# Optimization experiments

Measured on AMD Instinct MI355X. Metric: run time of the kernel, lower is better.

The kernel has to match this reference:

```python
import jax, jax.numpy as jnp
import numpy as np

B, S, D, H, W1, G = 2, 4096, 768, 12, 256, 8  # W1 = one-sided window (attention_window // 2)
HD = D // H
NC = S // W1  # number of query chunks of size W1
NEG = -1e9


def setup_inputs():
    key = jax.random.key(0)
    ks = jax.random.split(key, 9)
    def w(k):
        return jax.random.normal(k, (D, D), jnp.float32) * 0.02
    zb = jnp.zeros((D,), jnp.float32)
    # mask: >0 global, 0 local, <0 masked. First G tokens are global.
    mask = jnp.zeros((B, 1, 1, S), jnp.int32).at[:, :, :, :G].set(1)
    return {
        "hidden_states": jax.random.normal(ks[0], (B, S, D), jnp.float32),
        "attention_mask": mask,
        "Wq": w(ks[1]), "bq": zb,
        "Wk": w(ks[2]), "bk": zb,
        "Wv": w(ks[3]), "bv": zb,
        "Wqg": w(ks[4]), "bqg": zb,
        "Wkg": w(ks[5]), "bkg": zb,
        "Wvg": w(ks[6]), "bvg": zb,
        "Wo": w(ks[7]), "bo": zb,
        "n_global": G,
    }


def reference(hidden_states, attention_mask, Wq, bq, Wk, bk, Wv, bv,
              Wqg, bqg, Wkg, bkg, Wvg, bvg, Wo, bo, n_global):
    g = n_global
    mask = attention_mask.reshape(B, S)
    key_neg = mask < 0  # masked-out positions
    scale = 1.0 / np.sqrt(HD)

    def heads(x):  # [B,S,D] -> [B,H,S,HD]
        return x.reshape(B, S, H, HD).transpose(0, 2, 1, 3)

    q = heads(hidden_states @ Wq + bq) * scale
    k = heads(hidden_states @ Wk + bk)
    v = heads(hidden_states @ Wv + bv)

    # ---- sliding-window (banded) scores via 3-chunk gather ----
    idx = jnp.arange(NC)[:, None] * W1 + jnp.arange(3 * W1)[None, :]  # [NC,3W] into padded seq
    k_ch = jnp.pad(k, ((0, 0), (0, 0), (W1, W1), (0, 0)))[:, :, idx]  # [B,H,NC,3W,HD]
    q_ch = q.reshape(B, H, NC, W1, HD)
    band = jnp.einsum('bhcqd,bhckd->bhcqk', q_ch, k_ch)  # [B,H,NC,W,3W]

    qi = jnp.arange(W1)
    kj = jnp.arange(3 * W1)
    band_ok = jnp.abs(kj[None, :] - W1 - qi[:, None]) <= W1        # [W,3W] |j-i|<=w
    j_abs = idx - W1                                               # absolute key index
    in_range = (j_abs >= 0) & (j_abs < S)                          # [NC,3W]
    neg_ch = jnp.pad(key_neg, ((0, 0), (W1, W1)))[:, idx]          # [B,NC,3W]
    valid = (band_ok[None, None, None]
             & in_range[None, None, :, None, :]
             & (~neg_ch)[:, None, :, None, :])                     # [B,1,NC,W,3W]
    band = jnp.where(valid, band, NEG)

    # ---- scores of every query against the global keys (regular k proj) ----
    glob = jnp.einsum('bhsd,bhgd->bhsg', q, k[:, :, :g])           # [B,H,S,G]
    glob = jnp.where(key_neg[:, None, None, :g], NEG, glob)

    scores = jnp.concatenate([glob.reshape(B, H, NC, W1, g), band], axis=-1)
    probs = jax.nn.softmax(scores, axis=-1)
    probs = jnp.where(key_neg.reshape(B, 1, NC, W1, 1), 0.0, probs)  # zero masked query rows

    v_ch = jnp.pad(v, ((0, 0), (0, 0), (W1, W1), (0, 0)))[:, :, idx]
    out = jnp.einsum('bhcqk,bhckd->bhcqd', probs[..., g:], v_ch)
    out = out + jnp.einsum('bhcqg,bhgd->bhcqd', probs[..., :g], v[:, :, :g])
    out = out.reshape(B, H, S, HD)

    # ---- global tokens: full attention with dedicated global projections ----
    qg = heads(hidden_states @ Wqg + bqg)[:, :, :g] * scale        # [B,H,G,HD]
    kg = heads(hidden_states @ Wkg + bkg)
    vg = heads(hidden_states @ Wvg + bvg)
    gs = jnp.einsum('bhgd,bhsd->bhgs', qg, kg)                     # [B,H,G,S]
    gs = jnp.where(key_neg[:, None, None, :], NEG, gs)
    gp = jax.nn.softmax(gs, axis=-1)
    og = jnp.einsum('bhgs,bhsd->bhgd', gp, vg)
    out = out.at[:, :, :g].set(og)

    merged = out.transpose(0, 2, 1, 3).reshape(B, S, D)
    return merged @ Wo + bo  # outer output projection
```

## Files before the change

kernel.cpp:

```cpp
#include <hip/hip_runtime.h>

#define BB 2
#define SS 4096
#define DD 768
#define HH 12
#define HDD 64
#define W1C 256
#define NCC 16
#define GG 8

typedef unsigned short u16;
typedef __attribute__((ext_vector_type(4))) unsigned short u16x4;
typedef __attribute__((ext_vector_type(8))) unsigned short u16x8;
typedef __attribute__((ext_vector_type(8))) short s16x8;
typedef __attribute__((ext_vector_type(4))) float f32x4;

__device__ __forceinline__ float b2f(u16 u) {
  union { unsigned int i; float f; } v;
  v.i = ((unsigned int)u) << 16;
  return v.f;
}
__device__ __forceinline__ u16 f2b(float f) {
  union { float f; unsigned int i; } v;
  v.f = f;
  unsigned int r = v.i + 0x7FFFu + ((v.i >> 16) & 1u);
  return (u16)(r >> 16);
}
__device__ __forceinline__ float fexp2(float x) {
#if __has_builtin(__builtin_amdgcn_exp2f)
  return __builtin_amdgcn_exp2f(x);
#else
  return exp2f(x);
#endif
}
__device__ __forceinline__ unsigned pk_bf16(float lo, float hi) {
  unsigned r;
  asm("v_cvt_pk_bf16_f32 %0, %1, %2" : "=v"(r) : "v"(lo), "v"(hi));
  return r;
}
__device__ __forceinline__ void load_lds16(const void* g, void* l) {
  __builtin_amdgcn_global_load_lds(
      (const __attribute__((address_space(1))) unsigned int*)g,
      (__attribute__((address_space(3))) unsigned int*)l, 16, 0, 0);
}

#define QSCALE 0.18033688011112042f

__global__ __launch_bounds__(256) void cvt_f32_bf16(
    const float* __restrict__ in, u16* __restrict__ out, int n8) {
  int i = blockIdx.x * 256 + threadIdx.x;
  if (i >= n8) return;
  const float4* p = (const float4*)(in + (size_t)i * 8);
  float4 a = p[0], b = p[1];
  u16x8 o;
  o[0] = f2b(a.x); o[1] = f2b(a.y); o[2] = f2b(a.z); o[3] = f2b(a.w);
  o[4] = f2b(b.x); o[5] = f2b(b.y); o[6] = f2b(b.z); o[7] = f2b(b.w);
  *(u16x8*)(out + (size_t)i * 8) = o;
}

struct WtArgs { const float* W[6]; };

__global__ __launch_bounds__(256) void transpose_wt(WtArgs wa,
                                                    u16* __restrict__ WT) {
  __shared__ float T[64][65];
  const int mat = blockIdx.z;
  const int k0 = blockIdx.y * 64;
  const int n0 = blockIdx.x * 64;
  const float* __restrict__ W = wa.W[mat];
  const int t = threadIdx.x;
#pragma unroll
  for (int i = 0; i < 4; i++) {
    int idx4 = t + i * 256;
    int r = idx4 >> 4, c4 = idx4 & 15;
    float4 v = *(const float4*)(W + (size_t)(k0 + r) * 768 + n0 + c4 * 4);
    T[r][c4 * 4 + 0] = v.x; T[r][c4 * 4 + 1] = v.y;
    T[r][c4 * 4 + 2] = v.z; T[r][c4 * 4 + 3] = v.w;
  }
  __syncthreads();
#pragma unroll
  for (int i = 0; i < 2; i++) {
    int ci = t + i * 256;
    int nl = ci >> 3, k8 = ci & 7;
    u16x8 o;
#pragma unroll
    for (int jj = 0; jj < 8; jj++) o[jj] = f2b(T[k8 * 8 + jj][nl]);
    *(u16x8*)(WT + ((size_t)mat * 768 + n0 + nl) * 768 + k0 + k8 * 8) = o;
  }
}

struct BiasArgs { const float* bias[5]; };

template <int MODE>
__global__ __launch_bounds__(256) void gemm_bf16(
    const u16* __restrict__ A, const u16* __restrict__ WT, BiasArgs ba,
    u16* __restrict__ outb, float* __restrict__ outf) {
  __shared__ __align__(16) u16 As[128 * 64];
  __shared__ __align__(16) u16 Bs[128 * 64];
  const int tid = threadIdx.x;
  const int w = tid >> 6, l = tid & 63;
  const int lq = l & 15, g = l >> 4;

  const int NB = (MODE == 0) ? 30 : 6;
  const int nwg = NB * 64;
  const int cpx = nwg >> 3;
  const int id = (int)blockIdx.x;
  const int swz = (id & 7) * cpx + (id >> 3);
  const int bn = swz % NB, bm = swz / NB;

  const int m0 = bm * 128;
  const int wsel = (MODE == 0) ? (bn / 6) : 0;
  const int n0 = (MODE == 0) ? ((bn % 6) * 128) : (bn * 128);
  const int nw0 = bn * 128;
  const float* __restrict__ bias = ba.bias[wsel];
  const int wm = w >> 1, wn = w & 1;

  f32x4 acc[4][4];
#pragma unroll
  for (int i = 0; i < 4; i++)
#pragma unroll
    for (int j = 0; j < 4; j++) acc[i][j] = (f32x4){0.f, 0.f, 0.f, 0.f};

  for (int k0 = 0; k0 < 768; k0 += 64) {
    __syncthreads();
#pragma unroll
    for (int j = 0; j < 4; j++) {
      const int ci = (j * 4 + w) * 64 + l;
      const int row = ci >> 3, sl = ci & 7;
      const int src = sl ^ (row & 7);
      load_lds16(A + (size_t)(m0 + row) * 768 + k0 + src * 8,
                 (char*)As + (j * 4 + w) * 1024);
    }
#pragma unroll
    for (int j = 0; j < 4; j++) {
      const int ci = (j * 4 + w) * 64 + l;
      const int row = ci >> 3, sl = ci & 7;
      const int src = sl ^ (row & 7);
      load_lds16(WT + (size_t)(nw0 + row) * 768 + k0 + src * 8,
                 (char*)Bs + (j * 4 + w) * 1024);
    }
    asm volatile("s_waitcnt vmcnt(0)" ::: "memory");
    __syncthreads();
#pragma unroll
    for (int s = 0; s < 2; s++) {
      s16x8 af[4], bf[4];
#pragma unroll
      for (int mi = 0; mi < 4; mi++) {
        const int r = wm * 64 + mi * 16 + lq;
        af[mi] = *(const s16x8*)(As + r * 64 + (((s * 4 + g) ^ (r & 7)) * 8));
      }
#pragma unroll
      for (int nj = 0; nj < 4; nj++) {
        const int r = wn * 64 + nj * 16 + lq;
        bf[nj] = *(const s16x8*)(Bs + r * 64 + (((s * 4 + g) ^ (r & 7)) * 8));
      }
#pragma unroll
      for (int mi = 0; mi < 4; mi++)
#pragma unroll
        for (int nj = 0; nj < 4; nj++)
          acc[mi][nj] = __builtin_amdgcn_mfma_f32_16x16x32_bf16(
              af[mi], bf[nj], acc[mi][nj], 0, 0, 0);
    }
  }

  const int rbase = g * 4;
  const int cl = lq;
  if (MODE == 0) {
    const float scale = (wsel == 0) ? QSCALE : 1.0f;
    u16* outw = outb + (size_t)wsel * ((size_t)BB * HH * SS * HDD);
#pragma unroll
    for (int nj = 0; nj < 4; nj++) {
      const int c = n0 + wn * 64 + nj * 16 + cl;
      const float bv = bias[c];
      const int h = c >> 6, hd = c & 63;
#pragma unroll
      for (int mi = 0; mi < 4; mi++) {
#pragma unroll
        for (int r = 0; r < 4; r++) {
          const int m = m0 + wm * 64 + mi * 16 + rbase + r;
          const int b = m >> 12, s = m & 4095;
          outw[((size_t)(b * HH + h) * SS + s) * HDD + hd] =
              f2b((acc[mi][nj][r] + bv) * scale);
        }
      }
    }
  } else {
#pragma unroll
    for (int nj = 0; nj < 4; nj++) {
      const int c = n0 + wn * 64 + nj * 16 + cl;
      const float bv = bias[c];
#pragma unroll
      for (int mi = 0; mi < 4; mi++) {
#pragma unroll
        for (int r = 0; r < 4; r++) {
          const int m = m0 + wm * 64 + mi * 16 + rbase + r;
          outf[(size_t)m * 768 + c] = acc[mi][nj][r] + bv;
        }
      }
    }
  }
}

__global__ __launch_bounds__(256) void qg_proj(
    const float* __restrict__ hs, const float* __restrict__ Wqg,
    const float* __restrict__ bqg, u16* __restrict__ QG) {
  __shared__ float hsL[8][768];
  const int bh = blockIdx.x;
  const int b = bh / HH, h = bh % HH;
  const int t = threadIdx.x;
#pragma unroll
  for (int i = 0; i < 6; i++) {
    int idx = t + i * 256;
    int row = idx / 192, c4 = idx % 192;
    *(float4*)&hsL[row][c4 * 4] =
        *(const float4*)(hs + ((size_t)b * SS + row) * DD + c4 * 4);
  }
  __syncthreads();
#pragma unroll
  for (int rep = 0; rep < 2; rep++) {
    int qi = rep * 4 + (t >> 6);
    int d = t & 63, n = h * 64 + d;
    float acc = bqg[n];
    for (int k = 0; k < DD; k++)
      acc = fmaf(hsL[qi][k], Wqg[(size_t)k * DD + n], acc);
    QG[((size_t)bh * 16 + qi) * 64 + d] = f2b(acc * QSCALE);
  }
#pragma unroll
  for (int i = 0; i < 2; i++) {
    int idx = t + i * 256;
    int row = 8 + (idx >> 6), d = idx & 63;
    QG[((size_t)bh * 16 + row) * 64 + d] = 0;
  }
}

template <int GLOBAL>
__global__ __launch_bounds__(256) void attn_mfma(
    const u16* __restrict__ Q, const u16* __restrict__ K,
    const u16* __restrict__ V, const int* __restrict__ amask,
    u16* __restrict__ ATT, float* __restrict__ Pnum,
    float* __restrict__ Pden) {
  extern __shared__ __align__(16) char smem[];
  const int tid = threadIdx.x;
  const int w = tid >> 6, lane = tid & 63;
  const int lq = lane & 15, g = lane >> 4;
  const int h = blockIdx.y, b = blockIdx.z;
  const int bh = b * HH + h;
  const size_t bhs = (size_t)bh * SS;
  const int q0 = GLOBAL ? 0 : (int)blockIdx.x * 64;
  const int split = GLOBAL ? (int)blockIdx.x : 0;

  char* Kl;
  char* VT;
  if constexpr (GLOBAL) {
    Kl = smem + w * 16384;
    VT = Kl + 8192;
  } else {
    Kl = smem;
    VT = smem + 8192;
  }

  s16x8 qf[2];
  {
    const u16* qp = GLOBAL ? (Q + ((size_t)bh * 16 + lq) * 64)
                           : (Q + (bhs + q0 + w * 16 + lq) * 64);
    qf[0] = *(const s16x8*)(qp + g * 8);
    qf[1] = *(const s16x8*)(qp + 32 + g * 8);
  }

  f32x4 oacc[4];
#pragma unroll
  for (int i = 0; i < 4; i++) oacc[i] = (f32x4){0.f, 0.f, 0.f, 0.f};
  float denom = 0.f;

  const int NT = GLOBAL ? 2 : 10;
  for (int kt = 0; kt < NT; kt++) {
    int j0, klimit;
    bool bandfree;
    if constexpr (GLOBAL) {
      j0 = split * 512 + (w * 2 + kt) * 64;
      bandfree = true;
      klimit = 64;
    } else {
      if (kt < 9) { j0 = q0 - 256 + kt * 64; bandfree = false; klimit = 64; }
      else        { j0 = 0;                  bandfree = true;  klimit = 8; }
    }

    int jm = j0 + lane;
    int mv = ((unsigned)jm < (unsigned)SS) ? amask[b * SS + jm] : -1;
    bool okk = (mv >= 0) && (lane < klimit);
    unsigned long long vm = __ballot(okk);

    if constexpr (GLOBAL) {
      asm volatile("s_waitcnt lgkmcnt(0)" ::: "memory");
      const u16* Ks = K + bhs * 64 + (size_t)j0 * 64;
#pragma unroll
      for (int i = 0; i < 8; i++) {
        int ci = i * 64 + lane;
        int row = ci >> 3, cc = ci & 7, cs = cc ^ (row & 7);
        load_lds16(Ks + row * 64 + cs * 8, Kl + i * 1024);
      }
      const u16* Vs = V + bhs * 64 + (size_t)j0 * 64;
#pragma unroll
      for (int p = 0; p < 8; p++) {
        u16x8 vv = *(const u16x8*)(Vs + (size_t)lane * 64 + p * 8);
#pragma unroll
        for (int e = 0; e < 8; e++)
          *(u16*)(VT + (p * 8 + e) * 128 + ((lane * 2) ^ (e << 4))) = vv[e];
      }
      asm volatile("s_waitcnt vmcnt(0) lgkmcnt(0)" ::: "memory");
    } else {
      __syncthreads();
      if (j0 >= 0 && j0 + 64 <= SS) {
        const u16* Ks = K + bhs * 64 + (size_t)j0 * 64;
#pragma unroll
        for (int i = 0; i < 2; i++) {
          int ci = (i * 4 + w) * 64 + lane;
          int row = ci >> 3, cc = ci & 7, cs = cc ^ (row & 7);
          load_lds16(Ks + row * 64 + cs * 8, Kl + (i * 4 + w) * 1024);
        }
      } else {
#pragma unroll
        for (int i = 0; i < 2; i++) {
          int ci = (i * 4 + w) * 64 + lane;
          int row = ci >> 3, cc = ci & 7, cs = cc ^ (row & 7);
          int jj = j0 + row;
          u16x8 val;
#pragma unroll
          for (int e = 0; e < 8; e++) val[e] = 0;
          if ((unsigned)jj < (unsigned)SS)
            val = *(const u16x8*)(K + (bhs + jj) * 64 + cs * 8);
          *(u16x8*)(Kl + ci * 16) = val;
        }
      }
#pragma unroll
      for (int p = 0; p < 2; p++) {
        int d0 = p * 32 + w * 8;
        int jj = j0 + lane;
        u16x8 vv;
#pragma unroll
        for (int e = 0; e < 8; e++) vv[e] = 0;
        if ((unsigned)jj < (unsigned)SS)
          vv = *(const u16x8*)(V + (bhs + jj) * 64 + d0);
#pragma unroll
        for (int e = 0; e < 8; e++)
          *(u16*)(VT + (d0 + e) * 128 + ((lane * 2) ^ (e << 4))) = vv[e];
      }
      asm volatile("s_waitcnt vmcnt(0)" ::: "memory");
      __syncthreads();
    }

    f32x4 sc[4];
#pragma unroll
    for (int i = 0; i < 4; i++) sc[i] = (f32x4){0.f, 0.f, 0.f, 0.f};
#pragma unroll
    for (int s = 0; s < 2; s++) {
#pragma unroll
      for (int ks = 0; ks < 4; ks++) {
        s16x8 kf = *(const s16x8*)(Kl + (ks * 16 + lq) * 128 +
                                   (((s * 4 + g) ^ (lq & 7)) << 4));
        sc[ks] = __builtin_amdgcn_mfma_f32_16x16x32_bf16(kf, qf[s], sc[ks],
                                                          0, 0, 0);
      }
    }

    {
      const unsigned mlo = (unsigned)vm, mhi = (unsigned)(vm >> 32);
      const int q_abs = q0 + w * 16 + lq;
      bool allin = bandfree;
      if constexpr (!GLOBAL) {
        const int qw = q0 + w * 16;
        allin = bandfree || (j0 >= qw - 241 && j0 <= qw + 193);
      }
      const bool fast = (vm == ~0ull) && allin;
      const int ddq = j0 + g * 4 - q_abs;
      const int gsh = g * 4;
      if (fast) {
#pragma unroll
        for (int ks = 0; ks < 4; ks++)
#pragma unroll
          for (int r = 0; r < 4; r++) {
            float p = fexp2(sc[ks][r]);
            sc[ks][r] = p;
            denom += p;
          }
      } else {
#pragma unroll
        for (int ks = 0; ks < 4; ks++)
#pragma unroll
          for (int r = 0; r < 4; r++) {
            float e = fexp2(sc[ks][r]);
            unsigned bit =
                ((ks < 2 ? mlo : mhi) >> (gsh + ((ks & 1) * 16 + r))) & 1u;
            bool ok = bit && (allin ||
                              (unsigned)(ddq + ks * 16 + r + 256) <= 512u);
            float p = ok ? e : 0.f;
            sc[ks][r] = p;
            denom += p;
          }
      }
    }

#pragma unroll
    for (int s = 0; s < 2; s++) {
      const int srcA = lq + ((g & 1) << 5);
      const bool hiSel = g >= 2;
      float L[4], H[4];
#pragma unroll
      for (int r = 0; r < 4; r++) {
        float a0 = __shfl(sc[2 * s][r], srcA);
        float a1 = __shfl(sc[2 * s + 1][r], srcA);
        L[r] = hiSel ? a1 : a0;
        float b0 = __shfl(sc[2 * s][r], srcA + 16);
        float b1 = __shfl(sc[2 * s + 1][r], srcA + 16);
        H[r] = hiSel ? b1 : b0;
      }
      union { unsigned u[4]; s16x8 v; } pf;
      pf.u[0] = pk_bf16(L[0], L[1]);
      pf.u[1] = pk_bf16(L[2], L[3]);
      pf.u[2] = pk_bf16(H[0], H[1]);
      pf.u[3] = pk_bf16(H[2], H[3]);
#pragma unroll
      for (int dblk = 0; dblk < 4; dblk++) {
        s16x8 vf = *(const s16x8*)(VT + (dblk * 16 + lq) * 128 +
                                   (((s * 4 + g) ^ (lq & 7)) << 4));
        oacc[dblk] = __builtin_amdgcn_mfma_f32_16x16x32_bf16(vf, pf.v,
                                                              oacc[dblk],
                                                              0, 0, 0);
      }
    }
  }

  denom += __shfl_xor(denom, 16);
  denom += __shfl_xor(denom, 32);
  if constexpr (!GLOBAL) {
    const int q_abs = q0 + w * 16 + lq;
    const float rowscale = (amask[b * SS + q_abs] >= 0) ? (1.f / denom) : 0.f;
    u16* orow = ATT + ((size_t)b * SS + q_abs) * DD + h * 64;
#pragma unroll
    for (int dblk = 0; dblk < 4; dblk++) {
      u16x4 o;
#pragma unroll
      for (int r = 0; r < 4; r++) o[r] = f2b(oacc[dblk][r] * rowscale);
      *(u16x4*)(orow + dblk * 16 + g * 4) = o;
    }
  } else {
    const int pidx = split * 4 + w;
    float* np = Pnum + ((size_t)bh * 32 + pidx) * 1024;
#pragma unroll
    for (int dblk = 0; dblk < 4; dblk++)
#pragma unroll
      for (int r = 0; r < 4; r++)
        np[(dblk * 16 + g * 4 + r) * 16 + lq] = oacc[dblk][r];
    Pden[((size_t)bh * 32 + pidx) * 16 + lq] = denom;
  }
}

__global__ __launch_bounds__(512) void gmerge(const float* __restrict__ Pnum,
                                              const float* __restrict__ Pden,
                                              u16* __restrict__ ATT) {
  const int bh = blockIdx.x;
  const int b = bh / HH, h = bh % HH;
  const int t = threadIdx.x;
  const int q = t >> 6, d = t & 63;
  float num = 0.f, den = 0.f;
#pragma unroll 4
  for (int p = 0; p < 32; p++) {
    num += Pnum[((size_t)bh * 32 + p) * 1024 + d * 16 + q];
    den += Pden[((size_t)bh * 32 + p) * 16 + q];
  }
  ATT[((size_t)b * SS + q) * DD + h * 64 + d] = f2b(num / den);
}

extern "C" void kernel_launch(void* const* d_in, const int* in_sizes, int n_in,
                              void* d_out, int out_size, void* d_ws,
                              size_t ws_size, hipStream_t stream) {
  const float* hs = (const float*)d_in[0];
  const int* amask = (const int*)d_in[1];
  const float* Wq = (const float*)d_in[2];
  const float* bq = (const float*)d_in[3];
  const float* Wk = (const float*)d_in[4];
  const float* bk = (const float*)d_in[5];
  const float* Wv = (const float*)d_in[6];
  const float* bv = (const float*)d_in[7];
  const float* Wqg = (const float*)d_in[8];
  const float* bqg = (const float*)d_in[9];
  const float* Wkg = (const float*)d_in[10];
  const float* bkg = (const float*)d_in[11];
  const float* Wvg = (const float*)d_in[12];
  const float* bvg = (const float*)d_in[13];
  const float* Wo = (const float*)d_in[14];
  const float* bo = (const float*)d_in[15];
  float* out = (float*)d_out;

  char* ws = (char*)d_ws;
  const size_t QSZB = (size_t)BB * HH * SS * HDD * 2;
  u16* Qb = (u16*)(ws + 0);
  u16* Kb = (u16*)(ws + QSZB);
  u16* Vb = (u16*)(ws + 2 * QSZB);
  u16* KGb = (u16*)(ws + 3 * QSZB);
  u16* VGb = (u16*)(ws + 4 * QSZB);
  u16* Ab = (u16*)(ws + 5 * QSZB);
  u16* WTb = (u16*)(ws + 6 * QSZB);
  u16* ATTb = (u16*)(ws + 6 * QSZB + 7077888);
  u16* QGb = (u16*)(ws + 7 * QSZB + 7077888);
  float* Pnum = (float*)(ws + 7 * QSZB + 7077888 + 49152);
  float* Pden = (float*)(ws + 7 * QSZB + 7077888 + 49152 + 3145728);

  hipLaunchKernelGGL(cvt_f32_bf16, dim3(3072), dim3(256), 0, stream, hs, Ab,
                     (int)((size_t)BB * SS * DD / 8));

  WtArgs wa;
  wa.W[0] = Wq; wa.W[1] = Wk; wa.W[2] = Wv;
  wa.W[3] = Wkg; wa.W[4] = Wvg; wa.W[5] = Wo;
  hipLaunchKernelGGL(transpose_wt, dim3(12, 12, 6), dim3(256), 0, stream, wa,
                     WTb);

  BiasArgs b0;
  b0.bias[0] = bq; b0.bias[1] = bk; b0.bias[2] = bv;
  b0.bias[3] = bkg; b0.bias[4] = bvg;
  hipLaunchKernelGGL((gemm_bf16<0>), dim3(1920), dim3(256), 0, stream, Ab,
                     WTb, b0, Qb, (float*)nullptr);

  hipLaunchKernelGGL(qg_proj, dim3(24), dim3(256), 0, stream, hs, Wqg, bqg,
                     QGb);

  hipLaunchKernelGGL((attn_mfma<1>), dim3(8, HH, BB), dim3(256), 65536,
                     stream, QGb, KGb, VGb, amask, (u16*)nullptr, Pnum, Pden);

  hipLaunchKernelGGL((attn_mfma<0>), dim3(64, HH, BB), dim3(256), 16384,
                     stream, Qb, Kb, Vb, amask, ATTb, (float*)nullptr,
                     (float*)nullptr);

  hipLaunchKernelGGL(gmerge, dim3(24), dim3(512), 0, stream, Pnum, Pden, ATTb);

  BiasArgs b1;
  for (int i = 0; i < 5; i++) b1.bias[i] = bo;
  hipLaunchKernelGGL((gemm_bf16<1>), dim3(384), dim3(256), 0, stream, ATTb,
                     WTb + (size_t)5 * 768 * 768, b1, (u16*)nullptr, out);
}
```

Measured before the change: 208.9 us.

## Double-buffer bf16 GEMM with larger 256x256 tiles and 512-thread blocks

```diff
diff --git a/kernel.cpp b/kernel.cpp
--- a/kernel.cpp
+++ b/kernel.cpp
@@ -91,92 +91,149 @@
 struct BiasArgs { const float* bias[5]; };
 
 template <int MODE>
-__global__ __launch_bounds__(256) void gemm_bf16(
+__global__ __launch_bounds__(512, 1) void gemm_bf16(
     const u16* __restrict__ A, const u16* __restrict__ WT, BiasArgs ba,
     u16* __restrict__ outb, float* __restrict__ outf) {
-  __shared__ __align__(16) u16 As[128 * 64];
-  __shared__ __align__(16) u16 Bs[128 * 64];
+  constexpr int BM = (MODE == 0) ? 256 : 128;
+  constexpr int WM = BM / 2;
+  constexpr int MHAL = BM / 128;
+  constexpr int ATILE = BM * 64 * 2;
+  constexpr int BTILE = 256 * 64 * 2;
+  constexpr int BUFB = ATILE + BTILE;
+  constexpr int ACH = ATILE / 1024;
+  constexpr int ALD = ACH / 8;
+  constexpr int NTL = (MODE == 0) ? 15 : 3;
+  constexpr int NWG = (MODE == 0) ? 480 : 192;
+  constexpr int NT = 12;
+
+  extern __shared__ __align__(16) char smem[];
+
   const int tid = threadIdx.x;
   const int w = tid >> 6, l = tid & 63;
   const int lq = l & 15, g = l >> 4;
-
-  const int NB = (MODE == 0) ? 30 : 6;
-  const int nwg = NB * 64;
-  const int cpx = nwg >> 3;
+  const int wm = w >> 2, wn = w & 3;
+
+  const int cpx = NWG >> 3;
   const int id = (int)blockIdx.x;
   const int swz = (id & 7) * cpx + (id >> 3);
-  const int bn = swz % NB, bm = swz / NB;
-
-  const int m0 = bm * 128;
-  const int wsel = (MODE == 0) ? (bn / 6) : 0;
-  const int n0 = (MODE == 0) ? ((bn % 6) * 128) : (bn * 128);
-  const int nw0 = bn * 128;
+  const int bm = swz / NTL, bn = swz % NTL;
+  const int m0 = bm * BM;
+  const int nw0 = bn * 256;
+  const int wsel = (MODE == 0) ? (bn / 3) : 0;
+  const int nmat0 = (MODE == 0) ? ((bn % 3) * 256) : (bn * 256);
   const float* __restrict__ bias = ba.bias[wsel];
-  const int wm = w >> 1, wn = w & 1;
-
-  f32x4 acc[4][4];
-#pragma unroll
-  for (int i = 0; i < 4; i++)
+
+  f32x4 acc[MHAL * 4][4];
+#pragma unroll
+  for (int i = 0; i < MHAL * 4; i++)
 #pragma unroll
     for (int j = 0; j < 4; j++) acc[i][j] = (f32x4){0.f, 0.f, 0.f, 0.f};
 
-  for (int k0 = 0; k0 < 768; k0 += 64) {
-    __syncthreads();
+  auto stage = [&](int t) {
+    const int k0 = t * 64;
+    char* uA = smem + (t & 1) * BUFB;
+    char* uB = uA + ATILE;
+#pragma unroll
+    for (int j = 0; j < ALD; j++) {
+      const int ci = j * 8 + w;
+      const int p = ci * 64 + l;
+      const int row = p >> 3, sl = p & 7;
+      load_lds16(A + (size_t)(m0 + row) * 768 + k0 + ((sl ^ (row & 7)) * 8),
+                 uA + ci * 1024);
+    }
 #pragma unroll
     for (int j = 0; j < 4; j++) {
-      const int ci = (j * 4 + w) * 64 + l;
-      const int row = ci >> 3, sl = ci & 7;
-      const int src = sl ^ (row & 7);
-      load_lds16(A + (size_t)(m0 + row) * 768 + k0 + src * 8,
-                 (char*)As + (j * 4 + w) * 1024);
-    }
-#pragma unroll
-    for (int j = 0; j < 4; j++) {
-      const int ci = (j * 4 + w) * 64 + l;
-      const int row = ci >> 3, sl = ci & 7;
-      const int src = sl ^ (row & 7);
-      load_lds16(WT + (size_t)(nw0 + row) * 768 + k0 + src * 8,
-                 (char*)Bs + (j * 4 + w) * 1024);
-    }
-    asm volatile("s_waitcnt vmcnt(0)" ::: "memory");
-    __syncthreads();
-#pragma unroll
-    for (int s = 0; s < 2; s++) {
-      s16x8 af[4], bf[4];
-#pragma unroll
-      for (int mi = 0; mi < 4; mi++) {
-        const int r = wm * 64 + mi * 16 + lq;
-        af[mi] = *(const s16x8*)(As + r * 64 + (((s * 4 + g) ^ (r & 7)) * 8));
-      }
-#pragma unroll
-      for (int nj = 0; nj < 4; nj++) {
-        const int r = wn * 64 + nj * 16 + lq;
-        bf[nj] = *(const s16x8*)(Bs + r * 64 + (((s * 4 + g) ^ (r & 7)) * 8));
-      }
-#pragma unroll
-      for (int mi = 0; mi < 4; mi++)
-#pragma unroll
-        for (int nj = 0; nj < 4; nj++)
-          acc[mi][nj] = __builtin_amdgcn_mfma_f32_16x16x32_bf16(
-              af[mi], bf[nj], acc[mi][nj], 0, 0, 0);
-    }
-  }
-
-  const int rbase = g * 4;
-  const int cl = lq;
+      const int ci = j * 8 + w;
+      const int p = ci * 64 + l;
+      const int row = p >> 3, sl = p & 7;
+      load_lds16(WT + (size_t)(nw0 + row) * 768 + k0 + ((sl ^ (row & 7)) * 8),
+                 uB + ci * 1024);
+    }
+  };
+
+  stage(0);
+  stage(1);
+  if constexpr (MODE == 0)
+    asm volatile("s_waitcnt vmcnt(8)" ::: "memory");
+  else
+    asm volatile("s_waitcnt vmcnt(6)" ::: "memory");
+  __builtin_amdgcn_sched_barrier(0);
+  __builtin_amdgcn_s_barrier();
+  __builtin_amdgcn_sched_barrier(0);
+
+  for (int kt = 0; kt < NT; kt++) {
+    const int cur = kt & 1;
+    const u16* rA = (const u16*)(smem + cur * BUFB);
+    const u16* rB = (const u16*)(smem + cur * BUFB + ATILE);
+
+#pragma unroll
+    for (int nh = 0; nh < 2; nh++) {
+      s16x8 bf[2][2];
+#pragma unroll
+      for (int nj = 0; nj < 2; nj++) {
+        const int r = wn * 64 + (nh * 2 + nj) * 16 + lq;
+#pragma unroll
+        for (int ks = 0; ks < 2; ks++)
+          bf[nj][ks] =
+              *(const s16x8*)(rB + r * 64 + (((ks * 4 + g) ^ (r & 7)) * 8));
+      }
+#pragma unroll
+      for (int mh = 0; mh < MHAL; mh++) {
+        s16x8 af[4][2];
+#pragma unroll
+        for (int mi = 0; mi < 4; mi++) {
+          const int r = wm * WM + (mh * 4 + mi) * 16 + lq;
+#pragma unroll
+          for (int ks = 0; ks < 2; ks++)
+            af[mi][ks] =
+                *(const s16x8*)(rA + r * 64 + (((ks * 4 + g) ^ (r & 7)) * 8));
+        }
+        __builtin_amdgcn_s_setprio(1);
+#pragma unroll
+        for (int mi = 0; mi < 4; mi++)
+#pragma unroll
+          for (int nj = 0; nj < 2; nj++)
+#pragma unroll
+            for (int ks = 0; ks < 2; ks++)
+              acc[mh * 4 + mi][nh * 2 + nj] =
+                  __builtin_amdgcn_mfma_f32_16x16x32_bf16(
+                      af[mi][ks], bf[nj][ks], acc[mh * 4 + mi][nh * 2 + nj],
+                      0, 0, 0);
+        __builtin_amdgcn_s_setprio(0);
+      }
+    }
+
+    asm volatile("s_waitcnt lgkmcnt(0)" ::: "memory");
+    __builtin_amdgcn_sched_barrier(0);
+    __builtin_amdgcn_s_barrier();
+    __builtin_amdgcn_sched_barrier(0);
+    if (kt < NT - 2) stage(kt + 2);
+    if (kt < NT - 2) {
+      if constexpr (MODE == 0)
+        asm volatile("s_waitcnt vmcnt(8)" ::: "memory");
+      else
+        asm volatile("s_waitcnt vmcnt(6)" ::: "memory");
+    } else {
+      asm volatile("s_waitcnt vmcnt(0)" ::: "memory");
+    }
+    __builtin_amdgcn_sched_barrier(0);
+    __builtin_amdgcn_s_barrier();
+    __builtin_amdgcn_sched_barrier(0);
+  }
+
   if (MODE == 0) {
     const float scale = (wsel == 0) ? QSCALE : 1.0f;
     u16* outw = outb + (size_t)wsel * ((size_t)BB * HH * SS * HDD);
 #pragma unroll
     for (int nj = 0; nj < 4; nj++) {
-      const int c = n0 + wn * 64 + nj * 16 + cl;
+      const int c = nmat0 + wn * 64 + nj * 16 + lq;
       const float bv = bias[c];
       const int h = c >> 6, hd = c & 63;
 #pragma unroll
-      for (int mi = 0; mi < 4; mi++) {
+      for (int mi = 0; mi < MHAL * 4; mi++) {
 #pragma unroll
         for (int r = 0; r < 4; r++) {
-          const int m = m0 + wm * 64 + mi * 16 + rbase + r;
+          const int m = m0 + wm * WM + mi * 16 + g * 4 + r;
           const int b = m >> 12, s = m & 4095;
           outw[((size_t)(b * HH + h) * SS + s) * HDD + hd] =
               f2b((acc[mi][nj][r] + bv) * scale);
@@ -186,13 +243,13 @@
   } else {
 #pragma unroll
     for (int nj = 0; nj < 4; nj++) {
-      const int c = n0 + wn * 64 + nj * 16 + cl;
+      const int c = nmat0 + wn * 64 + nj * 16 + lq;
       const float bv = bias[c];
 #pragma unroll
-      for (int mi = 0; mi < 4; mi++) {
+      for (int mi = 0; mi < MHAL * 4; mi++) {
 #pragma unroll
         for (int r = 0; r < 4; r++) {
-          const int m = m0 + wm * 64 + mi * 16 + rbase + r;
+          const int m = m0 + wm * WM + mi * 16 + g * 4 + r;
           outf[(size_t)m * 768 + c] = acc[mi][nj][r] + bv;
         }
       }
@@ -517,8 +574,8 @@
   BiasArgs b0;
   b0.bias[0] = bq; b0.bias[1] = bk; b0.bias[2] = bv;
   b0.bias[3] = bkg; b0.bias[4] = bvg;
-  hipLaunchKernelGGL((gemm_bf16<0>), dim3(1920), dim3(256), 0, stream, Ab,
-                     WTb, b0, Qb, (float*)nullptr);
+  hipLaunchKernelGGL((gemm_bf16<0>), dim3(480), dim3(512), 131072, stream,
+                     Ab, WTb, b0, Qb, (float*)nullptr);
 
   hipLaunchKernelGGL(qg_proj, dim3(24), dim3(256), 0, stream, hs, Wqg, bqg,
                      QGb);
@@ -534,6 +591,7 @@
 
   BiasArgs b1;
   for (int i = 0; i < 5; i++) b1.bias[i] = bo;
-  hipLaunchKernelGGL((gemm_bf16<1>), dim3(384), dim3(256), 0, stream, ATTb,
-                     WTb + (size_t)5 * 768 * 768, b1, (u16*)nullptr, out);
-}
+  hipLaunchKernelGGL((gemm_bf16<1>), dim3(192), dim3(512), 98304, stream,
+                     ATTb, WTb + (size_t)5 * 768 * 768, b1, (u16*)nullptr,
+                     out);
+}
```

Result: no change. 209.3 us (+0.2%).
